# Kernel tuning notes

Hardware: AMD Instinct MI355X
Metric: run time of the kernel (lower is better)

The kernel has to match this reference:

```python
import jax, jax.numpy as jnp
import numpy as np

N_NODES = 50000
N_EDGES = 800000
D = 128
L = 3
BN_EPS = 1e-5


def _l2norm(x):
    # torch F.normalize(p=2, dim=-1): x / max(||x||, 1e-12)
    n = jnp.linalg.norm(x, axis=-1, keepdims=True)
    return x / jnp.maximum(n, 1e-12)


def setup_inputs() -> dict:
    key = jax.random.key(0)
    ks = jax.random.split(key, 5)
    x = jax.random.normal(ks[0], (N_NODES, D), dtype=jnp.float32)
    edge_index = jax.random.randint(ks[1], (2, N_EDGES), 0, N_NODES, dtype=jnp.int64)
    # stacked per-layer params; Linear stored as [in, out] (y = x @ W + b)
    W1 = jax.random.normal(ks[2], (L, D, D), dtype=jnp.float32) * 0.05
    W2 = jax.random.normal(ks[3], (L, D, D), dtype=jnp.float32) * 0.05
    b1 = jnp.zeros((L, D), jnp.float32)
    b2 = jnp.zeros((L, D), jnp.float32)
    gamma = jnp.ones((L, D), jnp.float32)
    beta = jnp.zeros((L, D), jnp.float32)
    eps = jnp.zeros((L,), jnp.float32)
    return {"x": x, "edge_index": edge_index, "W1": W1, "b1": b1,
            "gamma": gamma, "beta": beta, "W2": W2, "b2": b2, "eps": eps}


def _gin_layer(x, src, dst, W1, b1, g, be, W2, b2, eps):
    # message + scatter-add aggregation: sum_j x_j -> node i
    agg = jax.ops.segment_sum(x[src], dst, num_segments=N_NODES)
    # update(): L2 normalize aggregated messages
    agg = _l2norm(agg)
    # eps-weighted residual on L2-normalized root features
    out = agg + (1.0 + eps) * _l2norm(x)
    # MLP: Linear -> BatchNorm1d (training stats) -> ReLU -> Linear
    h = out @ W1 + b1
    mu = jnp.mean(h, axis=0)
    var = jnp.mean(jnp.square(h - mu), axis=0)  # biased var (torch BN training)
    h = g * (h - mu) * jax.lax.rsqrt(var + BN_EPS) + be
    h = jax.nn.relu(h)
    return h @ W2 + b2


def reference(x, edge_index, W1, b1, gamma, beta, W2, b2, eps):
    src, dst = edge_index[0], edge_index[1]
    for i in range(L):
        x = _gin_layer(x, src, dst, W1[i], b1[i], gamma[i], beta[i], W2[i], b2[i], eps[i])
        if i != L - 1:
            x = jax.nn.relu(x)
    return x
```

## Files before the change

kernel.cpp:

```cpp
#include <hip/hip_runtime.h>
#include <hip/hip_bf16.h>

#define N_NODES 50000
#define N_EDGES 800000
#define D 128
#define L_LAYERS 3
#define BN_EPS 1e-5f
#define NBUK 196
#define BIN_CHUNK 4096
#define NBIN_BLOCKS 196
#define BSTRIDE 5120
#define CSTRIDE 5376
#define AROW 68
#define NPART 8
#define PADOFF (N_NODES << 8)

typedef __attribute__((ext_vector_type(8))) short short8;
typedef __attribute__((ext_vector_type(4))) float floatx4;
typedef __attribute__((ext_vector_type(4))) unsigned short ushort4v;

__device__ __forceinline__ unsigned short f2bf(float f) {
    unsigned u = __builtin_bit_cast(unsigned, f);
    u += 0x7FFFu + ((u >> 16) & 1u);
    return (unsigned short)(u >> 16);
}
__device__ __forceinline__ float bf2f(unsigned short h) {
    unsigned u = ((unsigned)h) << 16;
    return __builtin_bit_cast(float, u);
}
__device__ __forceinline__ float bf2f_lo(unsigned p) {
    return __builtin_bit_cast(float, p << 16);
}
__device__ __forceinline__ float bf2f_hi(unsigned p) {
    return __builtin_bit_cast(float, p & 0xFFFF0000u);
}

__device__ __forceinline__ int edge_at(const void* ei, const int* flag64, long long i) {
    if (*flag64) return (int)((const long long*)ei)[i];
    return ((const int*)ei)[i];
}

__global__ __launch_bounds__(256) void prep_kernel(const float* __restrict__ x,
        const void* __restrict__ ei, int* __restrict__ flag,
        const float* __restrict__ W1, const float* __restrict__ W2,
        short* __restrict__ Wp, unsigned short* __restrict__ xb,
        unsigned* __restrict__ zreg, int zwords) {
    int bid = blockIdx.x;
    int t = threadIdx.x;
    if (bid == 0) {
        __shared__ int nz;
        if (t == 0) nz = 0;
        __syncthreads();
        if (((const int*)ei)[2 * t + 1] != 0) atomicAdd(&nz, 1);
        __syncthreads();
        if (t == 0) *flag = (nz == 0) ? 1 : 0;
        for (int i = t; i < zwords; i += 256) zreg[i] = 0u;
        if (t < 64) ((unsigned*)(xb + (size_t)N_NODES * D))[t] = 0u;
    } else if (bid <= 48) {
        int tid = (bid - 1) * 256 + t;
        int mat = tid >> 11;
        int t2 = tid & 2047;
        int kt = t2 >> 9;
        int nt = (t2 >> 6) & 7;
        int lane = t2 & 63;
        const float* W = (mat < 3) ? (W1 + (size_t)mat * D * D)
                                   : (W2 + (size_t)(mat - 3) * D * D);
        int kbase = kt * 32 + (lane >> 4) * 8;
        int n = nt * 16 + (lane & 15);
        short8 frag;
        #pragma unroll
        for (int j = 0; j < 8; j++) frag[j] = (short)f2bf(W[(kbase + j) * D + n]);
        *(short8*)(Wp + (size_t)mat * D * D + (size_t)t2 * 8) = frag;
    } else {
        long long i = (long long)((bid - 49) * 256 + t) * 4;
        float4 v = *(const float4*)(x + i);
        ushort4v o;
        o.x = f2bf(v.x); o.y = f2bf(v.y); o.z = f2bf(v.z); o.w = f2bf(v.w);
        *(ushort4v*)(xb + i) = o;
    }
}

__global__ __launch_bounds__(256) void bin_kernel(const void* __restrict__ ei,
        const int* __restrict__ flag64, int* __restrict__ bucketCursor,
        unsigned* __restrict__ binned) {
    __shared__ int lhist[NBUK];
    __shared__ int gbase[NBUK];
    int t = threadIdx.x;
    for (int i = t; i < NBUK; i += 256) lhist[i] = 0;
    __syncthreads();

    int e0 = blockIdx.x * BIN_CHUNK;
    unsigned w[BIN_CHUNK / 256];
    short bkt[BIN_CHUNK / 256];
    short lidx[BIN_CHUNK / 256];
    #pragma unroll
    for (int i = 0; i < BIN_CHUNK / 256; i++) {
        int e = e0 + t + i * 256;
        if (e < N_EDGES) {
            int s = edge_at(ei, flag64, e);
            int d = edge_at(ei, flag64, (long long)N_EDGES + e);
            int b = d >> 8;
            w[i] = ((unsigned)s << 8) | (unsigned)(d & 255);
            bkt[i] = (short)b;
            lidx[i] = (short)atomicAdd(&lhist[b], 1);
        } else {
            bkt[i] = -1;
        }
    }
    __syncthreads();
    for (int i = t; i < NBUK; i += 256) {
        int c = lhist[i];
        gbase[i] = i * BSTRIDE + (c ? atomicAdd(&bucketCursor[i], c) : 0);
    }
    __syncthreads();
    #pragma unroll
    for (int i = 0; i < BIN_CHUNK / 256; i++) {
        if (bkt[i] >= 0)
            binned[gbase[bkt[i]] + (int)lidx[i]] = w[i];
    }
}

__global__ __launch_bounds__(256) void csr_build_kernel(const unsigned* __restrict__ binned,
        const int* __restrict__ bucketCursor, int* __restrict__ rowptr,
        int* __restrict__ bucketEnd, int* __restrict__ csr) {
    __shared__ int ls[256];
    __shared__ int lhist[256];
    __shared__ int lcur[256];
    int b = blockIdx.x, t = threadIdx.x;
    int n = bucketCursor[b];
    const unsigned* src = binned + (size_t)b * BSTRIDE;

    lhist[t] = 0;
    __syncthreads();
    for (int i = t; i < n; i += 256)
        atomicAdd(&lhist[src[i] & 255u], 1);
    __syncthreads();
    int c = lhist[t];
    int pc = (c + 3) & ~3;
    ls[t] = pc;
    __syncthreads();
    for (int off = 1; off < 256; off <<= 1) {
        int u = (t >= off) ? ls[t - off] : 0;
        __syncthreads();
        ls[t] += u;
        __syncthreads();
    }
    int excl = ls[t] - pc;
    int base = b * CSTRIDE;
    int dst = b * 256 + t;
    if (dst <= N_NODES) rowptr[dst] = base + excl;
    if (t == 0) bucketEnd[b] = base + ls[255];
    lcur[t] = excl;
    __syncthreads();
    for (int i = t; i < n; i += 256) {
        unsigned wv = src[i];
        int pos = atomicAdd(&lcur[wv & 255u], 1);
        csr[base + pos] = (int)(wv & 0xFFFFFF00u);
    }
    __syncthreads();
    for (int i = lcur[t]; i < excl + pc; i++)
        csr[base + i] = PADOFF;
}

__global__ __launch_bounds__(256, 8) void gather_gemm1_kernel(
        const unsigned short* __restrict__ xb,
        const int* __restrict__ rowptr, const int* __restrict__ csr,
        const int* __restrict__ bucketEnd,
        const float* __restrict__ epsArr, int layer,
        const short* __restrict__ Wp, const float* __restrict__ bB,
        unsigned* __restrict__ Hout,
        float* __restrict__ gsum, float* __restrict__ gsq) {
    __shared__ __attribute__((aligned(16))) unsigned lA[16 * AROW];
    __shared__ int wq;
    const char* xbase = (const char*)xb;
    int wave = threadIdx.x >> 6, lane = threadIdx.x & 63;
    int g = lane >> 4, p = lane & 15;
    unsigned po = (unsigned)(p << 4);
    int r0 = blockIdx.x * 16;
    float eps1 = 1.0f + epsArr[layer];
    if (threadIdx.x == 0) wq = 0;
    __syncthreads();

    for (;;) {
        int r;
        if (lane == 0) r = atomicAdd(&wq, 1);
        r = __shfl(r, 0);
        if (r >= 16) break;
        int row = r0 + r;
        int beg = rowptr[row];
        int end = ((row & 255) == 255) ? bucketEnd[row >> 8] : rowptr[row + 1];
        float ac[8];
        #pragma unroll
        for (int k = 0; k < 8; k++) ac[k] = 0.f;
        for (int base = beg; base < end; base += 64) {
            int n = end - base;
            if (n > 64) n = 64;
            unsigned idxv = (lane < n) ? (unsigned)csr[base + lane] : (unsigned)PADOFF;
            int j = 0;
            for (; j + 8 <= n; j += 8) {
                unsigned o0 = (unsigned)__shfl((int)idxv, j + g) + po;
                unsigned o1 = (unsigned)__shfl((int)idxv, j + 4 + g) + po;
                uint4 v0 = *(const uint4*)(xbase + o0);
                uint4 v1 = *(const uint4*)(xbase + o1);
                ac[0] += bf2f_lo(v0.x); ac[1] += bf2f_hi(v0.x);
                ac[2] += bf2f_lo(v0.y); ac[3] += bf2f_hi(v0.y);
                ac[4] += bf2f_lo(v0.z); ac[5] += bf2f_hi(v0.z);
                ac[6] += bf2f_lo(v0.w); ac[7] += bf2f_hi(v0.w);
                ac[0] += bf2f_lo(v1.x); ac[1] += bf2f_hi(v1.x);
                ac[2] += bf2f_lo(v1.y); ac[3] += bf2f_hi(v1.y);
                ac[4] += bf2f_lo(v1.z); ac[5] += bf2f_hi(v1.z);
                ac[6] += bf2f_lo(v1.w); ac[7] += bf2f_hi(v1.w);
            }
            if (j < n) {
                unsigned o0 = (unsigned)__shfl((int)idxv, j + g) + po;
                uint4 v0 = *(const uint4*)(xbase + o0);
                ac[0] += bf2f_lo(v0.x); ac[1] += bf2f_hi(v0.x);
                ac[2] += bf2f_lo(v0.y); ac[3] += bf2f_hi(v0.y);
                ac[4] += bf2f_lo(v0.z); ac[5] += bf2f_hi(v0.z);
                ac[6] += bf2f_lo(v0.w); ac[7] += bf2f_hi(v0.w);
            }
        }
        #pragma unroll
        for (int k = 0; k < 8; k++) {
            ac[k] += __shfl_xor(ac[k], 16);
            ac[k] += __shfl_xor(ac[k], 32);
        }
        uint4 sv = *(const uint4*)(xbase + (((unsigned)row << 8) + po));
        float xv[8];
        xv[0] = bf2f_lo(sv.x); xv[1] = bf2f_hi(sv.x);
        xv[2] = bf2f_lo(sv.y); xv[3] = bf2f_hi(sv.y);
        xv[4] = bf2f_lo(sv.z); xv[5] = bf2f_hi(sv.z);
        xv[6] = bf2f_lo(sv.w); xv[7] = bf2f_hi(sv.w);
        float sa = 0.f, sx = 0.f;
        #pragma unroll
        for (int k = 0; k < 8; k++) { sa += ac[k] * ac[k]; sx += xv[k] * xv[k]; }
        #pragma unroll
        for (int mm = 8; mm >= 1; mm >>= 1) {
            sa += __shfl_xor(sa, mm);
            sx += __shfl_xor(sx, mm);
        }
        float ra = 1.0f / fmaxf(sqrtf(sa), 1e-12f);
        float rx = eps1 / fmaxf(sqrtf(sx), 1e-12f);
        unsigned wds[4];
        #pragma unroll
        for (int k = 0; k < 4; k++) {
            float lo = ac[2 * k] * ra + xv[2 * k] * rx;
            float hi = ac[2 * k + 1] * ra + xv[2 * k + 1] * rx;
            wds[k] = (unsigned)f2bf(lo) | ((unsigned)f2bf(hi) << 16);
        }
        if (g == 0)
            *(uint4*)(lA + r * AROW + p * 4) = make_uint4(wds[0], wds[1], wds[2], wds[3]);
    }
    __syncthreads();

    int m = p;
    int nt0 = wave * 2, nt1 = nt0 + 1;
    short8 afr[4];
    #pragma unroll
    for (int kt = 0; kt < 4; kt++)
        afr[kt] = *(const short8*)(lA + m * AROW + kt * 16 + g * 4);
    __syncthreads();

    floatx4 acc0 = (floatx4){0.f, 0.f, 0.f, 0.f};
    floatx4 acc1 = (floatx4){0.f, 0.f, 0.f, 0.f};
    #pragma unroll
    for (int kt = 0; kt < 4; kt++) {
        short8 bf0 = *(const short8*)(Wp + (size_t)((kt * 8 + nt0) * 64 + lane) * 8);
        short8 bf1 = *(const short8*)(Wp + (size_t)((kt * 8 + nt1) * 64 + lane) * 8);
        acc0 = __builtin_amdgcn_mfma_f32_16x16x32_bf16(afr[kt], bf0, acc0, 0, 0, 0);
        acc1 = __builtin_amdgcn_mfma_f32_16x16x32_bf16(afr[kt], bf1, acc1, 0, 0, 0);
    }

    unsigned short* hlds = (unsigned short*)lA;
    float bc0 = bB[nt0 * 16 + m], bc1 = bB[nt1 * 16 + m];
    float s0 = 0.f, q0 = 0.f, s1 = 0.f, q1 = 0.f;
    #pragma unroll
    for (int r = 0; r < 4; r++) {
        int lrow = g * 4 + r;
        float h0 = acc0[r] + bc0;
        float h1 = acc1[r] + bc1;
        hlds[lrow * (AROW * 2) + nt0 * 16 + m] = f2bf(h0);
        hlds[lrow * (AROW * 2) + nt1 * 16 + m] = f2bf(h1);
        s0 += h0; q0 += h0 * h0;
        s1 += h1; q1 += h1 * h1;
    }
    s0 += __shfl_xor(s0, 16); s0 += __shfl_xor(s0, 32);
    q0 += __shfl_xor(q0, 16); q0 += __shfl_xor(q0, 32);
    s1 += __shfl_xor(s1, 16); s1 += __shfl_xor(s1, 32);
    q1 += __shfl_xor(q1, 16); q1 += __shfl_xor(q1, 32);
    if (lane < 16) {
        float* gs = gsum + (size_t)(blockIdx.x & (NPART - 1)) * D;
        float* gq = gsq + (size_t)(blockIdx.x & (NPART - 1)) * D;
        atomicAdd(&gs[nt0 * 16 + m], s0);
        atomicAdd(&gs[nt1 * 16 + m], s1);
        atomicAdd(&gq[nt0 * 16 + m], q0);
        atomicAdd(&gq[nt1 * 16 + m], q1);
    }
    __syncthreads();

    {
        int crow = threadIdx.x >> 4;
        int cq = threadIdx.x & 15;
        uint4 v = *(const uint4*)(lA + crow * AROW + cq * 4);
        *(uint4*)(Hout + (size_t)(r0 + crow) * 64 + cq * 4) = v;
    }
}

__global__ __launch_bounds__(256) void gemm2_mfma_kernel(const unsigned short* __restrict__ H,
        const float* __restrict__ gsum, const float* __restrict__ gsq,
        const float* __restrict__ gamma, const float* __restrict__ beta,
        const short* __restrict__ Wp, const float* __restrict__ b,
        float* __restrict__ Yf32, unsigned* __restrict__ Yb16, int finalLayer) {
    __shared__ float s_scale[D];
    __shared__ float s_shift[D];
    __shared__ unsigned so[64 * 132];
    if (threadIdx.x < D) {
        int c = threadIdx.x;
        const float invN = 1.0f / (float)N_NODES;
        float su = 0.f, sq = 0.f;
        #pragma unroll
        for (int pp = 0; pp < NPART; pp++) {
            su += gsum[(size_t)pp * D + c];
            sq += gsq[(size_t)pp * D + c];
        }
        float mu = su * invN;
        float var = fmaxf(sq * invN - mu * mu, 0.f);
        float is = rsqrtf(var + BN_EPS);
        float sc = gamma[c] * is;
        s_scale[c] = sc;
        s_shift[c] = beta[c] - mu * sc;
    }
    __syncthreads();

    int wave = threadIdx.x >> 6, lane = threadIdx.x & 63;
    int r0 = blockIdx.x * 64;
    int m = lane & 15, g = lane >> 4;
    int arow = r0 + wave * 16 + m;
    bool valid = arow < N_NODES;

    short8 a[4];
    #pragma unroll
    for (int kt = 0; kt < 4; kt++) {
        int koff = kt * 32 + g * 8;
        if (valid) {
            short8 hv = *(const short8*)(H + (long long)arow * D + koff);
            #pragma unroll
            for (int j = 0; j < 8; j++) {
                float h = bf2f((unsigned short)hv[j]);
                float v = fmaxf(h * s_scale[koff + j] + s_shift[koff + j], 0.f);
                a[kt][j] = (short)f2bf(v);
            }
        } else {
            a[kt] = (short8)0;
        }
    }

    floatx4 acc[8];
    #pragma unroll
    for (int nt = 0; nt < 8; nt++) acc[nt] = (floatx4){0.f, 0.f, 0.f, 0.f};

    #pragma unroll
    for (int nt = 0; nt < 8; nt++) {
        #pragma unroll
        for (int kt = 0; kt < 4; kt++) {
            short8 bf = *(const short8*)(Wp + (size_t)((kt * 8 + nt) * 64 + lane) * 8);
            acc[nt] = __builtin_amdgcn_mfma_f32_16x16x32_bf16(a[kt], bf, acc[nt], 0, 0, 0);
        }
    }

    if (finalLayer) {
        float* sof = (float*)so;
        #pragma unroll
        for (int nt = 0; nt < 8; nt++) {
            int col = nt * 16 + m;
            float bcol = b[col];
            #pragma unroll
            for (int r = 0; r < 4; r++) {
                int lrow = wave * 16 + g * 4 + r;
                sof[lrow * 132 + col] = acc[nt][r] + bcol;
            }
        }
        __syncthreads();
        #pragma unroll
        for (int k = 0; k < 8; k++) {
            int c = threadIdx.x + k * 256;
            int crow = c >> 5;
            int cq = c & 31;
            if (r0 + crow < N_NODES) {
                float4 v = *(const float4*)(sof + crow * 132 + cq * 4);
                *(float4*)(Yf32 + (size_t)(r0 + crow) * D + cq * 4) = v;
            }
        }
    } else {
        unsigned short* sos = (unsigned short*)so;
        #pragma unroll
        for (int nt = 0; nt < 8; nt++) {
            int col = nt * 16 + m;
            float bcol = b[col];
            #pragma unroll
            for (int r = 0; r < 4; r++) {
                int lrow = wave * 16 + g * 4 + r;
                sos[lrow * (AROW * 2) + col] = f2bf(fmaxf(acc[nt][r] + bcol, 0.f));
            }
        }
        __syncthreads();
        #pragma unroll
        for (int k = 0; k < 4; k++) {
            int c = threadIdx.x + k * 256;
            int crow = c >> 4;
            int cq = c & 15;
            if (r0 + crow < N_NODES) {
                uint4 v = *(const uint4*)(so + crow * AROW + cq * 4);
                *(uint4*)(Yb16 + (size_t)(r0 + crow) * 64 + cq * 4) = v;
            }
        }
    }
}

extern "C" void kernel_launch(void* const* d_in, const int* in_sizes, int n_in,
                              void* d_out, int out_size, void* d_ws, size_t ws_size,
                              hipStream_t stream) {
    const float* x      = (const float*)d_in[0];
    const void*  ei     = d_in[1];
    const float* W1     = (const float*)d_in[2];
    const float* b1     = (const float*)d_in[3];
    const float* gamma  = (const float*)d_in[4];
    const float* beta   = (const float*)d_in[5];
    const float* W2     = (const float*)d_in[6];
    const float* b2     = (const float*)d_in[7];
    const float* epsArr = (const float*)d_in[8];
    float* out = (float*)d_out;

    char* ws = (char*)d_ws;
    const size_t xbuf = (size_t)(N_NODES + 1) * D * sizeof(short);
    const size_t hbuf = (size_t)N_NODES * D * sizeof(short);
    unsigned short* Xb  = (unsigned short*)ws;
    unsigned* H16       = (unsigned*)(ws + xbuf);
    char* p             = ws + xbuf + hbuf;
    short* Wp       = (short*)p;         p += 6 * (size_t)D * D * sizeof(short);
    int* rowptr     = (int*)p;           p += (N_NODES + 1) * sizeof(int);
    int* csr        = (int*)p;           p += (size_t)NBUK * CSTRIDE * sizeof(int);
    unsigned* binned= (unsigned*)p;      p += (size_t)NBUK * BSTRIDE * sizeof(unsigned);
    int* bucketEnd  = (int*)p;           p += NBUK * sizeof(int);
    int* flag       = (int*)p;           p += sizeof(int);
    char* zbase     = p;
    int* bucketCursor=(int*)p;           p += NBUK * sizeof(int);
    float* stats    = (float*)p;         p += (size_t)L_LAYERS * 2 * NPART * D * sizeof(float);
    int zwords      = (int)((p - zbase) / 4);

    prep_kernel<<<1 + 48 + (N_NODES * D / 4) / 256, 256, 0, stream>>>(
        x, ei, flag, W1, W2, Wp, Xb, (unsigned*)zbase, zwords);

    bin_kernel<<<NBIN_BLOCKS, 256, 0, stream>>>(ei, flag, bucketCursor, binned);
    csr_build_kernel<<<NBUK, 256, 0, stream>>>(binned, bucketCursor, rowptr, bucketEnd, csr);

    const int g1Grid = N_NODES / 16;
    const int g2Grid = (N_NODES + 63) / 64;
    for (int l = 0; l < L_LAYERS; l++) {
        int fin = (l == L_LAYERS - 1) ? 1 : 0;
        float* gsum = stats + (size_t)l * 2 * NPART * D;
        float* gsq  = gsum + (size_t)NPART * D;

        gather_gemm1_kernel<<<g1Grid, 256, 0, stream>>>(
            Xb, rowptr, csr, bucketEnd, epsArr, l,
            Wp + (size_t)l * D * D, b1 + (size_t)l * D,
            H16, gsum, gsq);
        gemm2_mfma_kernel<<<g2Grid, 256, 0, stream>>>(
            (const unsigned short*)H16, gsum, gsq,
            gamma + (size_t)l * D, beta + (size_t)l * D,
            Wp + (size_t)(3 + l) * D * D, b2 + (size_t)l * D,
            out, (unsigned*)Xb, fin);
    }
}
```

Measured before the change: 210.3 us.

## Restructure edge gather per-lane, use packed bf16 convert, split final gemm2 kernel

```diff
diff --git a/kernel.cpp b/kernel.cpp
--- a/kernel.cpp
+++ b/kernel.cpp
@@ -17,7 +17,7 @@
 
 typedef __attribute__((ext_vector_type(8))) short short8;
 typedef __attribute__((ext_vector_type(4))) float floatx4;
-typedef __attribute__((ext_vector_type(4))) unsigned short ushort4v;
+typedef __attribute__((ext_vector_type(4))) unsigned uintx4;
 
 __device__ __forceinline__ unsigned short f2bf(float f) {
     unsigned u = __builtin_bit_cast(unsigned, f);
@@ -33,6 +33,11 @@
 }
 __device__ __forceinline__ float bf2f_hi(unsigned p) {
     return __builtin_bit_cast(float, p & 0xFFFF0000u);
+}
+__device__ __forceinline__ unsigned cvtpk(float lo, float hi) {
+    unsigned r;
+    asm("v_cvt_pk_bf16_f32 %0, %1, %2" : "=v"(r) : "v"(lo), "v"(hi));
+    return r;
 }
 
 __device__ __forceinline__ int edge_at(const void* ei, const int* flag64, long long i) {
@@ -67,16 +72,18 @@
                                    : (W2 + (size_t)(mat - 3) * D * D);
         int kbase = kt * 32 + (lane >> 4) * 8;
         int n = nt * 16 + (lane & 15);
-        short8 frag;
-        #pragma unroll
-        for (int j = 0; j < 8; j++) frag[j] = (short)f2bf(W[(kbase + j) * D + n]);
-        *(short8*)(Wp + (size_t)mat * D * D + (size_t)t2 * 8) = frag;
+        unsigned fw[4];
+        #pragma unroll
+        for (int j = 0; j < 4; j++)
+            fw[j] = cvtpk(W[(kbase + 2 * j) * D + n], W[(kbase + 2 * j + 1) * D + n]);
+        *(uint4*)(Wp + (size_t)mat * D * D + (size_t)t2 * 8) =
+            make_uint4(fw[0], fw[1], fw[2], fw[3]);
     } else {
         long long i = (long long)((bid - 49) * 256 + t) * 4;
         float4 v = *(const float4*)(x + i);
-        ushort4v o;
-        o.x = f2bf(v.x); o.y = f2bf(v.y); o.z = f2bf(v.z); o.w = f2bf(v.w);
-        *(ushort4v*)(xb + i) = o;
+        unsigned w0 = cvtpk(v.x, v.y);
+        unsigned w1 = cvtpk(v.z, v.w);
+        *(uint2*)(xb + i) = make_uint2(w0, w1);
     }
 }
 
@@ -174,12 +181,25 @@
     __shared__ int wq;
     const char* xbase = (const char*)xb;
     int wave = threadIdx.x >> 6, lane = threadIdx.x & 63;
-    int g = lane >> 4, p = lane & 15;
-    unsigned po = (unsigned)(p << 4);
+    unsigned po = (unsigned)(lane << 2);
     int r0 = blockIdx.x * 16;
     float eps1 = 1.0f + epsArr[layer];
     if (threadIdx.x == 0) wq = 0;
     __syncthreads();
+
+#define EDGE4(J) { \
+    unsigned o0 = (unsigned)__shfl((int)iv, (J) + 0) + po; \
+    unsigned o1 = (unsigned)__shfl((int)iv, (J) + 1) + po; \
+    unsigned o2 = (unsigned)__shfl((int)iv, (J) + 2) + po; \
+    unsigned o3 = (unsigned)__shfl((int)iv, (J) + 3) + po; \
+    unsigned p0 = *(const unsigned*)(xbase + o0); \
+    unsigned p1 = *(const unsigned*)(xbase + o1); \
+    unsigned p2 = *(const unsigned*)(xbase + o2); \
+    unsigned p3 = *(const unsigned*)(xbase + o3); \
+    a0 += bf2f_lo(p0); a1 += bf2f_hi(p0); \
+    b0 += bf2f_lo(p1); b1 += bf2f_hi(p1); \
+    c0 += bf2f_lo(p2); c1 += bf2f_hi(p2); \
+    d0 += bf2f_lo(p3); d1 += bf2f_hi(p3); }
 
     for (;;) {
         int r;
@@ -189,71 +209,39 @@
         int row = r0 + r;
         int beg = rowptr[row];
         int end = ((row & 255) == 255) ? bucketEnd[row >> 8] : rowptr[row + 1];
-        float ac[8];
-        #pragma unroll
-        for (int k = 0; k < 8; k++) ac[k] = 0.f;
+        float a0 = 0.f, a1 = 0.f, b0 = 0.f, b1 = 0.f;
+        float c0 = 0.f, c1 = 0.f, d0 = 0.f, d1 = 0.f;
         for (int base = beg; base < end; base += 64) {
             int n = end - base;
             if (n > 64) n = 64;
-            unsigned idxv = (lane < n) ? (unsigned)csr[base + lane] : (unsigned)PADOFF;
+            unsigned iv = (lane < n) ? (unsigned)csr[base + lane] : (unsigned)PADOFF;
             int j = 0;
-            for (; j + 8 <= n; j += 8) {
-                unsigned o0 = (unsigned)__shfl((int)idxv, j + g) + po;
-                unsigned o1 = (unsigned)__shfl((int)idxv, j + 4 + g) + po;
-                uint4 v0 = *(const uint4*)(xbase + o0);
-                uint4 v1 = *(const uint4*)(xbase + o1);
-                ac[0] += bf2f_lo(v0.x); ac[1] += bf2f_hi(v0.x);
-                ac[2] += bf2f_lo(v0.y); ac[3] += bf2f_hi(v0.y);
-                ac[4] += bf2f_lo(v0.z); ac[5] += bf2f_hi(v0.z);
-                ac[6] += bf2f_lo(v0.w); ac[7] += bf2f_hi(v0.w);
-                ac[0] += bf2f_lo(v1.x); ac[1] += bf2f_hi(v1.x);
-                ac[2] += bf2f_lo(v1.y); ac[3] += bf2f_hi(v1.y);
-                ac[4] += bf2f_lo(v1.z); ac[5] += bf2f_hi(v1.z);
-                ac[6] += bf2f_lo(v1.w); ac[7] += bf2f_hi(v1.w);
+            for (; j + 16 <= n; j += 16) {
+                EDGE4(j) EDGE4(j + 4) EDGE4(j + 8) EDGE4(j + 12)
             }
-            if (j < n) {
-                unsigned o0 = (unsigned)__shfl((int)idxv, j + g) + po;
-                uint4 v0 = *(const uint4*)(xbase + o0);
-                ac[0] += bf2f_lo(v0.x); ac[1] += bf2f_hi(v0.x);
-                ac[2] += bf2f_lo(v0.y); ac[3] += bf2f_hi(v0.y);
-                ac[4] += bf2f_lo(v0.z); ac[5] += bf2f_hi(v0.z);
-                ac[6] += bf2f_lo(v0.w); ac[7] += bf2f_hi(v0.w);
+            for (; j < n; j += 4) {
+                EDGE4(j)
             }
         }
-        #pragma unroll
-        for (int k = 0; k < 8; k++) {
-            ac[k] += __shfl_xor(ac[k], 16);
-            ac[k] += __shfl_xor(ac[k], 32);
-        }
-        uint4 sv = *(const uint4*)(xbase + (((unsigned)row << 8) + po));
-        float xv[8];
-        xv[0] = bf2f_lo(sv.x); xv[1] = bf2f_hi(sv.x);
-        xv[2] = bf2f_lo(sv.y); xv[3] = bf2f_hi(sv.y);
-        xv[4] = bf2f_lo(sv.z); xv[5] = bf2f_hi(sv.z);
-        xv[6] = bf2f_lo(sv.w); xv[7] = bf2f_hi(sv.w);
-        float sa = 0.f, sx = 0.f;
-        #pragma unroll
-        for (int k = 0; k < 8; k++) { sa += ac[k] * ac[k]; sx += xv[k] * xv[k]; }
-        #pragma unroll
-        for (int mm = 8; mm >= 1; mm >>= 1) {
+        float ax = a0 + b0 + c0 + d0;
+        float ay = a1 + b1 + c1 + d1;
+        unsigned pself = *(const unsigned*)(xbase + (((unsigned)row << 8) + po));
+        float xv0 = bf2f_lo(pself), xv1 = bf2f_hi(pself);
+        float sa = ax * ax + ay * ay;
+        float sx = xv0 * xv0 + xv1 * xv1;
+        #pragma unroll
+        for (int mm = 32; mm >= 1; mm >>= 1) {
             sa += __shfl_xor(sa, mm);
             sx += __shfl_xor(sx, mm);
         }
         float ra = 1.0f / fmaxf(sqrtf(sa), 1e-12f);
         float rx = eps1 / fmaxf(sqrtf(sx), 1e-12f);
-        unsigned wds[4];
-        #pragma unroll
-        for (int k = 0; k < 4; k++) {
-            float lo = ac[2 * k] * ra + xv[2 * k] * rx;
-            float hi = ac[2 * k + 1] * ra + xv[2 * k + 1] * rx;
-            wds[k] = (unsigned)f2bf(lo) | ((unsigned)f2bf(hi) << 16);
-        }
-        if (g == 0)
-            *(uint4*)(lA + r * AROW + p * 4) = make_uint4(wds[0], wds[1], wds[2], wds[3]);
-    }
-    __syncthreads();
-
-    int m = p;
+        lA[r * AROW + lane] = cvtpk(ax * ra + xv0 * rx, ay * ra + xv1 * rx);
+    }
+#undef EDGE4
+    __syncthreads();
+
+    int m = lane & 15, g = lane >> 4;
     int nt0 = wave * 2, nt1 = nt0 + 1;
     short8 afr[4];
     #pragma unroll
@@ -306,14 +294,14 @@
     }
 }
 
-__global__ __launch_bounds__(256) void gemm2_mfma_kernel(const unsigned short* __restrict__ H,
+__global__ __launch_bounds__(256, 8) void gemm2_mid_kernel(const unsigned short* __restrict__ H,
         const float* __restrict__ gsum, const float* __restrict__ gsq,
         const float* __restrict__ gamma, const float* __restrict__ beta,
         const short* __restrict__ Wp, const float* __restrict__ b,
-        float* __restrict__ Yf32, unsigned* __restrict__ Yb16, int finalLayer) {
+        unsigned* __restrict__ Yb16) {
     __shared__ float s_scale[D];
     __shared__ float s_shift[D];
-    __shared__ unsigned so[64 * 132];
+    __shared__ unsigned so[64 * AROW];
     if (threadIdx.x < D) {
         int c = threadIdx.x;
         const float invN = 1.0f / (float)N_NODES;
@@ -344,12 +332,16 @@
         int koff = kt * 32 + g * 8;
         if (valid) {
             short8 hv = *(const short8*)(H + (long long)arow * D + koff);
+            unsigned aw[4];
             #pragma unroll
-            for (int j = 0; j < 8; j++) {
-                float h = bf2f((unsigned short)hv[j]);
-                float v = fmaxf(h * s_scale[koff + j] + s_shift[koff + j], 0.f);
-                a[kt][j] = (short)f2bf(v);
+            for (int jj = 0; jj < 4; jj++) {
+                float h0 = bf2f((unsigned short)hv[2 * jj]);
+                float h1 = bf2f((unsigned short)hv[2 * jj + 1]);
+                float v0 = fmaxf(h0 * s_scale[koff + 2 * jj] + s_shift[koff + 2 * jj], 0.f);
+                float v1 = fmaxf(h1 * s_scale[koff + 2 * jj + 1] + s_shift[koff + 2 * jj + 1], 0.f);
+                aw[jj] = cvtpk(v0, v1);
             }
+            a[kt] = __builtin_bit_cast(short8, (uintx4){aw[0], aw[1], aw[2], aw[3]});
         } else {
             a[kt] = (short8)0;
         }
@@ -358,7 +350,6 @@
     floatx4 acc[8];
     #pragma unroll
     for (int nt = 0; nt < 8; nt++) acc[nt] = (floatx4){0.f, 0.f, 0.f, 0.f};
-
     #pragma unroll
     for (int nt = 0; nt < 8; nt++) {
         #pragma unroll
@@ -368,51 +359,114 @@
         }
     }
 
-    if (finalLayer) {
-        float* sof = (float*)so;
-        #pragma unroll
-        for (int nt = 0; nt < 8; nt++) {
-            int col = nt * 16 + m;
-            float bcol = b[col];
+    unsigned short* sos = (unsigned short*)so;
+    #pragma unroll
+    for (int nt = 0; nt < 8; nt++) {
+        int col = nt * 16 + m;
+        float bcol = b[col];
+        #pragma unroll
+        for (int r = 0; r < 4; r++) {
+            int lrow = wave * 16 + g * 4 + r;
+            sos[lrow * (AROW * 2) + col] = f2bf(fmaxf(acc[nt][r] + bcol, 0.f));
+        }
+    }
+    __syncthreads();
+    #pragma unroll
+    for (int k = 0; k < 4; k++) {
+        int c = threadIdx.x + k * 256;
+        int crow = c >> 4;
+        int cq = c & 15;
+        if (r0 + crow < N_NODES) {
+            uint4 v = *(const uint4*)(so + crow * AROW + cq * 4);
+            *(uint4*)(Yb16 + (size_t)(r0 + crow) * 64 + cq * 4) = v;
+        }
+    }
+}
+
+__global__ __launch_bounds__(256, 4) void gemm2_final_kernel(const unsigned short* __restrict__ H,
+        const float* __restrict__ gsum, const float* __restrict__ gsq,
+        const float* __restrict__ gamma, const float* __restrict__ beta,
+        const short* __restrict__ Wp, const float* __restrict__ b,
+        float* __restrict__ Yf32) {
+    __shared__ float s_scale[D];
+    __shared__ float s_shift[D];
+    __shared__ float sof[64 * 132];
+    if (threadIdx.x < D) {
+        int c = threadIdx.x;
+        const float invN = 1.0f / (float)N_NODES;
+        float su = 0.f, sq = 0.f;
+        #pragma unroll
+        for (int pp = 0; pp < NPART; pp++) {
+            su += gsum[(size_t)pp * D + c];
+            sq += gsq[(size_t)pp * D + c];
+        }
+        float mu = su * invN;
+        float var = fmaxf(sq * invN - mu * mu, 0.f);
+        float is = rsqrtf(var + BN_EPS);
+        float sc = gamma[c] * is;
+        s_scale[c] = sc;
+        s_shift[c] = beta[c] - mu * sc;
+    }
+    __syncthreads();
+
+    int wave = threadIdx.x >> 6, lane = threadIdx.x & 63;
+    int r0 = blockIdx.x * 64;
+    int m = lane & 15, g = lane >> 4;
+    int arow = r0 + wave * 16 + m;
+    bool valid = arow < N_NODES;
+
+    short8 a[4];
+    #pragma unroll
+    for (int kt = 0; kt < 4; kt++) {
+        int koff = kt * 32 + g * 8;
+        if (valid) {
+            short8 hv = *(const short8*)(H + (long long)arow * D + koff);
+            unsigned aw[4];
             #pragma unroll
-            for (int r = 0; r < 4; r++) {
-                int lrow = wave * 16 + g * 4 + r;
-                sof[lrow * 132 + col] = acc[nt][r] + bcol;
+            for (int jj = 0; jj < 4; jj++) {
+                float h0 = bf2f((unsigned short)hv[2 * jj]);
+                float h1 = bf2f((unsigned short)hv[2 * jj + 1]);
+                float v0 = fmaxf(h0 * s_scale[koff + 2 * jj] + s_shift[koff + 2 * jj], 0.f);
+                float v1 = fmaxf(h1 * s_scale[koff + 2 * jj + 1] + s_shift[koff + 2 * jj + 1], 0.f);
+                aw[jj] = cvtpk(v0, v1);
             }
-        }
-        __syncthreads();
-        #pragma unroll
-        for (int k = 0; k < 8; k++) {
-            int c = threadIdx.x + k * 256;
-            int crow = c >> 5;
-            int cq = c & 31;
-            if (r0 + crow < N_NODES) {
-                float4 v = *(const float4*)(sof + crow * 132 + cq * 4);
-                *(float4*)(Yf32 + (size_t)(r0 + crow) * D + cq * 4) = v;
-            }
-        }
-    } else {
-        unsigned short* sos = (unsigned short*)so;
-        #pragma unroll
-        for (int nt = 0; nt < 8; nt++) {
-            int col = nt * 16 + m;
-            float bcol = b[col];
-            #pragma unroll
-            for (int r = 0; r < 4; r++) {
-                int lrow = wave * 16 + g * 4 + r;
-                sos[lrow * (AROW * 2) + col] = f2bf(fmaxf(acc[nt][r] + bcol, 0.f));
-            }
-        }
-        __syncthreads();
-        #pragma unroll
-        for (int k = 0; k < 4; k++) {
-            int c = threadIdx.x + k * 256;
-            int crow = c >> 4;
-            int cq = c & 15;
-            if (r0 + crow < N_NODES) {
-                uint4 v = *(const uint4*)(so + crow * AROW + cq * 4);
-                *(uint4*)(Yb16 + (size_t)(r0 + crow) * 64 + cq * 4) = v;
-            }
+            a[kt] = __builtin_bit_cast(short8, (uintx4){aw[0], aw[1], aw[2], aw[3]});
+        } else {
+            a[kt] = (short8)0;
+        }
+    }
+
+    floatx4 acc[8];
+    #pragma unroll
+    for (int nt = 0; nt < 8; nt++) acc[nt] = (floatx4){0.f, 0.f, 0.f, 0.f};
+    #pragma unroll
+    for (int nt = 0; nt < 8; nt++) {
+        #pragma unroll
+        for (int kt = 0; kt < 4; kt++) {
+            short8 bf = *(const short8*)(Wp + (size_t)((kt * 8 + nt) * 64 + lane) * 8);
+            acc[nt] = __builtin_amdgcn_mfma_f32_16x16x32_bf16(a[kt], bf, acc[nt], 0, 0, 0);
+        }
+    }
+
+    #pragma unroll
+    for (int nt = 0; nt < 8; nt++) {
+        int col = nt * 16 + m;
+        float bcol = b[col];
+        #pragma unroll
+        for (int r = 0; r < 4; r++) {
+            int lrow = wave * 16 + g * 4 + r;
+            sof[lrow * 132 + col] = acc[nt][r] + bcol;
+        }
+    }
+    __syncthreads();
+    #pragma unroll
+    for (int k = 0; k < 8; k++) {
+        int c = threadIdx.x + k * 256;
+        int crow = c >> 5;
+        int cq = c & 31;
+        if (r0 + crow < N_NODES) {
+            float4 v = *(const float4*)(sof + crow * 132 + cq * 4);
+            *(float4*)(Yf32 + (size_t)(r0 + crow) * D + cq * 4) = v;
         }
     }
 }
@@ -457,7 +511,6 @@
     const int g1Grid = N_NODES / 16;
     const int g2Grid = (N_NODES + 63) / 64;
     for (int l = 0; l < L_LAYERS; l++) {
-        int fin = (l == L_LAYERS - 1) ? 1 : 0;
         float* gsum = stats + (size_t)l * 2 * NPART * D;
         float* gsq  = gsum + (size_t)NPART * D;
 
@@ -465,10 +518,16 @@
             Xb, rowptr, csr, bucketEnd, epsArr, l,
             Wp + (size_t)l * D * D, b1 + (size_t)l * D,
             H16, gsum, gsq);
-        gemm2_mfma_kernel<<<g2Grid, 256, 0, stream>>>(
-            (const unsigned short*)H16, gsum, gsq,
-            gamma + (size_t)l * D, beta + (size_t)l * D,
-            Wp + (size_t)(3 + l) * D * D, b2 + (size_t)l * D,
-            out, (unsigned*)Xb, fin);
-    }
-}
+        if (l == L_LAYERS - 1) {
+            gemm2_final_kernel<<<g2Grid, 256, 0, stream>>>(
+                (const unsigned short*)H16, gsum, gsq,
+                gamma + (size_t)l * D, beta + (size_t)l * D,
+                Wp + (size_t)(3 + l) * D * D, b2 + (size_t)l * D, out);
+        } else {
+            gemm2_mid_kernel<<<g2Grid, 256, 0, stream>>>(
+                (const unsigned short*)H16, gsum, gsq,
+                gamma + (size_t)l * D, beta + (size_t)l * D,
+                Wp + (size_t)(3 + l) * D * D, b2 + (size_t)l * D, (unsigned*)Xb);
+        }
+    }
+}
```

Result: slower. 219.7 us (+4.5%).
